# Performance work log

Measured on AMD Instinct MI355X. Metric: run time of the kernel, lower is better.

## Reference

```python
import jax, jax.numpy as jnp
import numpy as np
import math

H = 32           # num heads
D_NOPE = 128
D_ROPE = 64
D_V = 128
HID = 4096
FFN = 16384
SEQ = 2048
B = 1
ROPE_BASE = 10000.0
EPS = 1e-6


def _layernorm(x, w, b):
    mu = jnp.mean(x, axis=-1, keepdims=True)
    var = jnp.var(x, axis=-1, keepdims=True)
    return (x - mu) * jax.lax.rsqrt(var + EPS) * w + b


def _rope(x):
    # x: [B, S, H, D_ROPE]; standard half-split rotary, positions = arange(S)
    S = x.shape[1]
    half = D_ROPE // 2
    inv_freq = 1.0 / (ROPE_BASE ** (jnp.arange(0, D_ROPE, 2, dtype=jnp.float32) / D_ROPE))  # [half]
    t = jnp.arange(S, dtype=jnp.float32)
    freqs = t[:, None] * inv_freq[None, :]           # [S, half]
    cos = jnp.cos(freqs)[None, :, None, :]           # [1, S, 1, half]
    sin = jnp.sin(freqs)[None, :, None, :]
    x1, x2 = x[..., :half], x[..., half:]
    return jnp.concatenate([x1 * cos - x2 * sin, x1 * sin + x2 * cos], axis=-1)


def setup_inputs() -> dict:
    key = jax.random.key(0)
    ks = jax.random.split(key, 8)
    std = 0.02
    hidden_states = jax.random.normal(ks[0], (B, SEQ, HID), dtype=jnp.float32)
    # causal additive mask
    causal = jnp.triu(jnp.full((SEQ, SEQ), -1e9, dtype=jnp.float32), k=1)
    attention_mask = causal[None, None, :, :]
    q_size = H * (D_NOPE + D_ROPE)
    w_q = jax.random.normal(ks[1], (q_size, HID), dtype=jnp.float32) * std
    w_k = jax.random.normal(ks[2], (q_size, HID), dtype=jnp.float32) * std
    w_v = jax.random.normal(ks[3], (H * D_V, HID), dtype=jnp.float32) * std
    w_o = jax.random.normal(ks[4], (HID, H * D_V), dtype=jnp.float32) * std
    w1 = jax.random.normal(ks[5], (FFN, HID), dtype=jnp.float32) * std
    w2 = jax.random.normal(ks[6], (HID, FFN), dtype=jnp.float32) * std
    ln1_w = jnp.ones((HID,), jnp.float32); ln1_b = jnp.zeros((HID,), jnp.float32)
    ln2_w = jnp.ones((HID,), jnp.float32); ln2_b = jnp.zeros((HID,), jnp.float32)
    return dict(hidden_states=hidden_states, attention_mask=attention_mask,
                w_q=w_q, w_k=w_k, w_v=w_v, w_o=w_o,
                ln1_w=ln1_w, ln1_b=ln1_b, ln2_w=ln2_w, ln2_b=ln2_b,
                w1=w1, w2=w2)


def reference(hidden_states, attention_mask, w_q, w_k, w_v, w_o,
              ln1_w, ln1_b, ln2_w, ln2_b, w1, w2):
    x = hidden_states
    b, s, _ = x.shape
    # --- attention block ---
    h = _layernorm(x, ln1_w, ln1_b)
    q = h @ w_q.T   # [b, s, H*(nope+rope)]
    k = h @ w_k.T
    v = (h @ w_v.T).reshape(b, s, H, D_V)
    q_nope = q[..., :H * D_NOPE].reshape(b, s, H, D_NOPE)
    q_rope = q[..., H * D_NOPE:].reshape(b, s, H, D_ROPE)
    k_nope = k[..., :H * D_NOPE].reshape(b, s, H, D_NOPE)
    k_rope = k[..., H * D_NOPE:].reshape(b, s, H, D_ROPE)
    q_rope = _rope(q_rope)
    k_rope = _rope(k_rope)
    scores = (jnp.einsum('bqhd,bkhd->bhqk', q_nope, k_nope) / math.sqrt(D_NOPE)
              + jnp.einsum('bqhd,bkhd->bhqk', q_rope, k_rope) / math.sqrt(D_ROPE))
    scores = scores + attention_mask
    attn = jax.nn.softmax(scores, axis=-1)
    ctx = jnp.einsum('bhqk,bkhd->bqhd', attn, v).reshape(b, s, H * D_V)
    attn_out = ctx @ w_o.T
    x = x + attn_out
    # --- FFN block (silu MLP) ---
    h2 = _layernorm(x, ln2_w, ln2_b)
    ffn = jax.nn.silu(h2 @ w1.T) @ w2.T
    return x + ffn
```

## Files before the change

### kernel.cpp

```cpp
#include <hip/hip_runtime.h>

typedef _Float16 f16x8 __attribute__((ext_vector_type(8)));
typedef _Float16 f16x4 __attribute__((ext_vector_type(4)));
typedef float f32x4 __attribute__((ext_vector_type(4)));

#define HID 4096
#define QDIM 6144
#define SEQ 2048
#define NH 32

__global__ __launch_bounds__(256) void ln_k(const float* __restrict__ x,
    const float* __restrict__ w, const float* __restrict__ b,
    _Float16* __restrict__ out)
{
    __shared__ float red[8];
    const int tid = threadIdx.x;
    const int row = blockIdx.x;
    const float* xr = x + (size_t)row * HID;
    float4 v[4];
    float s = 0.f, ss = 0.f;
#pragma unroll
    for (int i = 0; i < 4; i++) {
        v[i] = ((const float4*)xr)[i * 256 + tid];
        s  += v[i].x + v[i].y + v[i].z + v[i].w;
        ss += v[i].x * v[i].x + v[i].y * v[i].y + v[i].z * v[i].z + v[i].w * v[i].w;
    }
#pragma unroll
    for (int o = 1; o < 64; o <<= 1) { s += __shfl_xor(s, o); ss += __shfl_xor(ss, o); }
    if ((tid & 63) == 0) { red[tid >> 6] = s; red[4 + (tid >> 6)] = ss; }
    __syncthreads();
    s  = red[0] + red[1] + red[2] + red[3];
    ss = red[4] + red[5] + red[6] + red[7];
    const float mu = s * (1.f / HID);
    const float rstd = rsqrtf(ss * (1.f / HID) - mu * mu + 1e-6f);
    _Float16* orow = out + (size_t)row * HID;
#pragma unroll
    for (int i = 0; i < 4; i++) {
        int base = (i * 256 + tid) * 4;
        float vv[4] = { v[i].x, v[i].y, v[i].z, v[i].w };
#pragma unroll
        for (int c = 0; c < 4; c++)
            orow[base + c] = (_Float16)((vv[c] - mu) * rstd * w[base + c] + b[base + c]);
    }
}

template<int EPI>
__global__ __launch_bounds__(256) void gemm_k(const _Float16* __restrict__ A,
    const float* __restrict__ W, int N, int K,
    _Float16* __restrict__ o16, const float* __restrict__ resid,
    float* __restrict__ of)
{
    __shared__ _Float16 As[128 * 40];
    __shared__ _Float16 Ws[128 * 40];
    const int tid  = threadIdx.x;
    const int lane = tid & 63, wid = tid >> 6;
    const int l15  = lane & 15, quad = lane >> 4;
    const int wr   = wid >> 1,  wc   = wid & 1;
    const int m0 = blockIdx.x * 128, n0 = blockIdx.y * 128;

    f32x4 acc[4][4] = {};
    for (int k0 = 0; k0 < K; k0 += 32) {
        __syncthreads();
#pragma unroll
        for (int it = 0, c = tid; it < 2; it++, c += 256) {
            int row = c >> 2, col = (c & 3) << 3;
            f16x8 v = *(const f16x8*)(A + (size_t)(m0 + row) * K + k0 + col);
            *(f16x8*)(As + row * 40 + col) = v;
        }
#pragma unroll
        for (int it = 0, c = tid; it < 4; it++, c += 256) {
            int row = c >> 3, col = (c & 7) << 2;
            float4 wv = *(const float4*)(W + (size_t)(n0 + row) * K + k0 + col);
            f16x4 hv = { (_Float16)wv.x, (_Float16)wv.y, (_Float16)wv.z, (_Float16)wv.w };
            *(f16x4*)(Ws + row * 40 + col) = hv;
        }
        __syncthreads();
        f16x8 a[4], b[4];
#pragma unroll
        for (int i = 0; i < 4; i++)
            a[i] = *(const f16x8*)(As + (wr * 64 + i * 16 + l15) * 40 + quad * 8);
#pragma unroll
        for (int j = 0; j < 4; j++)
            b[j] = *(const f16x8*)(Ws + (wc * 64 + j * 16 + l15) * 40 + quad * 8);
#pragma unroll
        for (int i = 0; i < 4; i++)
#pragma unroll
            for (int j = 0; j < 4; j++)
                acc[i][j] = __builtin_amdgcn_mfma_f32_16x16x32_f16(a[i], b[j], acc[i][j], 0, 0, 0);
    }
#pragma unroll
    for (int i = 0; i < 4; i++) {
#pragma unroll
        for (int j = 0; j < 4; j++) {
#pragma unroll
            for (int r = 0; r < 4; r++) {
                int rg = m0 + wr * 64 + i * 16 + quad * 4 + r;
                int cg = n0 + wc * 64 + j * 16 + l15;
                size_t idx = (size_t)rg * N + cg;
                float cv = acc[i][j][r];
                if (EPI == 0)      o16[idx] = (_Float16)cv;
                else if (EPI == 1) o16[idx] = (_Float16)(cv / (1.f + __expf(-cv)));
                else               of[idx]  = resid[idx] + cv;
            }
        }
    }
}

__global__ __launch_bounds__(256) void rope_k(_Float16* __restrict__ q,
                                              _Float16* __restrict__ k)
{
    const int s = blockIdx.x, tid = threadIdx.x;
    _Float16* qr = q + (size_t)s * QDIM;
    _Float16* kr = k + (size_t)s * QDIM;
    const float scn = 0.08838834764831845f;
#pragma unroll
    for (int it = 0, c = tid; it < 2; it++, c += 256) {
        f16x8 v = *(const f16x8*)(qr + c * 8);
#pragma unroll
        for (int e = 0; e < 8; e++) v[e] = (_Float16)((float)v[e] * scn);
        *(f16x8*)(qr + c * 8) = v;
    }
#pragma unroll
    for (int it = 0, c = tid; it < 4; it++, c += 256) {
        int hh = c >> 5, i = c & 31;
        float invf = exp2f(-(float)i * 0.41524101186092029f);
        float ang = (float)s * invf;
        float co = cosf(ang), si = sinf(ang);
        int base = HID + hh * 64 + i;
        {
            float x1 = (float)qr[base], x2 = (float)qr[base + 32];
            qr[base]      = (_Float16)((x1 * co - x2 * si) * 0.125f);
            qr[base + 32] = (_Float16)((x1 * si + x2 * co) * 0.125f);
        }
        {
            float x1 = (float)kr[base], x2 = (float)kr[base + 32];
            kr[base]      = (_Float16)(x1 * co - x2 * si);
            kr[base + 32] = (_Float16)(x1 * si + x2 * co);
        }
    }
}

__global__ __launch_bounds__(256) void attn_k(const _Float16* __restrict__ qb,
    const _Float16* __restrict__ kb, const _Float16* __restrict__ vb,
    _Float16* __restrict__ ctxb)
{
    __shared__ _Float16 Ks[64 * 200];
    __shared__ _Float16 Vt[128 * 72];
    __shared__ _Float16 Ps[4][16 * 72];
    const int q0 = blockIdx.x * 64;
    const int h  = blockIdx.y;
    const int tid = threadIdx.x, lane = tid & 63, wid = tid >> 6;
    const int l15 = lane & 15, quad = lane >> 4;

    f16x8 aq[6];
    {
        const _Float16* qrow = qb + (size_t)(q0 + wid * 16 + l15) * QDIM;
#pragma unroll
        for (int c = 0; c < 6; c++) {
            int colb = (c < 4) ? (h * 128 + c * 32) : (HID + h * 64 + (c - 4) * 32);
            aq[c] = *(const f16x8*)(qrow + colb + quad * 8);
        }
    }
    f32x4 oacc[8] = {};
    float mrun[4] = { -1e30f, -1e30f, -1e30f, -1e30f };
    float lrun[4] = { 0.f, 0.f, 0.f, 0.f };

    const int nk = blockIdx.x + 1;
    for (int kt = 0; kt < nk; kt++) {
        const int k0 = kt * 64;
        __syncthreads();
        for (int c = tid; c < 1536; c += 256) {
            int f8 = c % 24, row = c / 24;
            int f = f8 << 3;
            int col = (f < 128) ? (h * 128 + f) : (HID + h * 64 + (f - 128));
            f16x8 v = *(const f16x8*)(kb + (size_t)(k0 + row) * QDIM + col);
            *(f16x8*)(Ks + row * 200 + f) = v;
        }
        for (int c = tid; c < 1024; c += 256) {
            int kl = c & 63, d8 = c >> 6;
            f16x8 v = *(const f16x8*)(vb + (size_t)(k0 + kl) * HID + h * 128 + (d8 << 3));
#pragma unroll
            for (int e = 0; e < 8; e++) Vt[(d8 * 8 + e) * 72 + kl] = v[e];
        }
        __syncthreads();
        f32x4 sa[4];
#pragma unroll
        for (int nt = 0; nt < 4; nt++) {
            f32x4 acc = {};
#pragma unroll
            for (int c = 0; c < 6; c++) {
                f16x8 bk = *(const f16x8*)(Ks + (nt * 16 + l15) * 200 + c * 32 + quad * 8);
                acc = __builtin_amdgcn_mfma_f32_16x16x32_f16(aq[c], bk, acc, 0, 0, 0);
            }
            sa[nt] = acc;
        }
#pragma unroll
        for (int r = 0; r < 4; r++) {
            const int qrow = q0 + wid * 16 + quad * 4 + r;
            float mx = -1e30f;
#pragma unroll
            for (int nt = 0; nt < 4; nt++) {
                int kcol = k0 + nt * 16 + l15;
                float sv = (kcol <= qrow) ? sa[nt][r] : -1e30f;
                sa[nt][r] = sv;
                mx = fmaxf(mx, sv);
            }
#pragma unroll
            for (int o = 1; o < 16; o <<= 1) mx = fmaxf(mx, __shfl_xor(mx, o));
            float mnew = fmaxf(mrun[r], mx);
            float alpha = __expf(mrun[r] - mnew);
            mrun[r] = mnew;
            float sum = 0.f;
#pragma unroll
            for (int nt = 0; nt < 4; nt++) {
                float p = __expf(sa[nt][r] - mnew);
                sa[nt][r] = p;
                sum += p;
            }
#pragma unroll
            for (int o = 1; o < 16; o <<= 1) sum += __shfl_xor(sum, o);
            lrun[r] = lrun[r] * alpha + sum;
#pragma unroll
            for (int ot = 0; ot < 8; ot++) oacc[ot][r] *= alpha;
#pragma unroll
            for (int nt = 0; nt < 4; nt++)
                Ps[wid][(quad * 4 + r) * 72 + nt * 16 + l15] = (_Float16)sa[nt][r];
        }
#pragma unroll
        for (int kc = 0; kc < 2; kc++) {
            f16x8 ap = *(const f16x8*)(&Ps[wid][l15 * 72 + kc * 32 + quad * 8]);
#pragma unroll
            for (int ot = 0; ot < 8; ot++) {
                f16x8 bv = *(const f16x8*)(Vt + (ot * 16 + l15) * 72 + kc * 32 + quad * 8);
                oacc[ot] = __builtin_amdgcn_mfma_f32_16x16x32_f16(ap, bv, oacc[ot], 0, 0, 0);
            }
        }
    }
#pragma unroll
    for (int r = 0; r < 4; r++) {
        const int srow = q0 + wid * 16 + quad * 4 + r;
        const float inv = 1.0f / lrun[r];
#pragma unroll
        for (int ot = 0; ot < 8; ot++)
            ctxb[(size_t)srow * HID + h * 128 + ot * 16 + l15] = (_Float16)(oacc[ot][r] * inv);
    }
}

extern "C" void kernel_launch(void* const* d_in, const int* in_sizes, int n_in,
                              void* d_out, int out_size, void* d_ws, size_t ws_size,
                              hipStream_t stream)
{
    const float* x   = (const float*)d_in[0];
    const float* wq  = (const float*)d_in[2];
    const float* wk  = (const float*)d_in[3];
    const float* wv  = (const float*)d_in[4];
    const float* wo  = (const float*)d_in[5];
    const float* l1w = (const float*)d_in[6];
    const float* l1b = (const float*)d_in[7];
    const float* l2w = (const float*)d_in[8];
    const float* l2b = (const float*)d_in[9];
    const float* w1  = (const float*)d_in[10];
    const float* w2  = (const float*)d_in[11];
    float* out = (float*)d_out;

    _Float16* ws   = (_Float16*)d_ws;
    _Float16* hb   = ws;
    _Float16* qb   = ws + 8388608;
    _Float16* kb   = qb + 12582912;
    _Float16* vb   = kb + 12582912;
    _Float16* ctxb = vb + 8388608;
    _Float16* h2b  = hb;
    _Float16* f1b  = qb;

    ln_k<<<SEQ, 256, 0, stream>>>(x, l1w, l1b, hb);
    gemm_k<0><<<dim3(16, 48),  256, 0, stream>>>(hb, wq, QDIM, HID, qb, nullptr, nullptr);
    gemm_k<0><<<dim3(16, 48),  256, 0, stream>>>(hb, wk, QDIM, HID, kb, nullptr, nullptr);
    gemm_k<0><<<dim3(16, 32),  256, 0, stream>>>(hb, wv, HID,  HID, vb, nullptr, nullptr);
    rope_k<<<SEQ, 256, 0, stream>>>(qb, kb);
    attn_k<<<dim3(32, NH), 256, 0, stream>>>(qb, kb, vb, ctxb);
    gemm_k<2><<<dim3(16, 32),  256, 0, stream>>>(ctxb, wo, HID, HID, nullptr, x, out);
    ln_k<<<SEQ, 256, 0, stream>>>(out, l2w, l2b, h2b);
    gemm_k<1><<<dim3(16, 128), 256, 0, stream>>>(h2b, w1, 16384, HID, f1b, nullptr, nullptr);
    gemm_k<2><<<dim3(16, 32),  256, 0, stream>>>(f1b, w2, HID, 16384, nullptr, out, out);
}
```

Before: 2.715 ms.

## Pre-convert weights to fp16, fuse QKV GEMM, use direct-to-LDS loads with swizzle

When the workspace is large enough, weights are converted to fp16 in separate kernels and Q/K/V are computed by one fused GEMM into an interleaved QKV buffer. The GEMM now uses global_load_lds direct-to-LDS copies with an XOR swizzle, a K-step of 64, and an XCD-aware block remapping. Otherwise it reads fp32 weights into LDS and converts on read. The goal is to cut the per-tile fp32 conversion and register staging overhead, at the cost of extra conversion passes over the weights each call.

```diff
diff --git a/kernel.cpp b/kernel.cpp
--- a/kernel.cpp
+++ b/kernel.cpp
@@ -5,9 +5,25 @@
 typedef float f32x4 __attribute__((ext_vector_type(4)));
 
 #define HID 4096
-#define QDIM 6144
 #define SEQ 2048
 #define NH 32
+#define QKVS 16384
+
+__device__ __forceinline__ void load_lds16(const void* g, void* l) {
+    __builtin_amdgcn_global_load_lds((const __attribute__((address_space(1))) void*)g,
+                                     (__attribute__((address_space(3))) void*)l, 16, 0, 0);
+}
+
+__global__ __launch_bounds__(256) void conv_k(const float* __restrict__ s,
+                                              _Float16* __restrict__ d)
+{
+    size_t i = ((size_t)blockIdx.x * 256 + threadIdx.x) * 8;
+    float4 a = *(const float4*)(s + i);
+    float4 b = *(const float4*)(s + i + 4);
+    f16x8 o = { (_Float16)a.x, (_Float16)a.y, (_Float16)a.z, (_Float16)a.w,
+                (_Float16)b.x, (_Float16)b.y, (_Float16)b.z, (_Float16)b.w };
+    *(f16x8*)(d + i) = o;
+}
 
 __global__ __launch_bounds__(256) void ln_k(const float* __restrict__ x,
     const float* __restrict__ w, const float* __restrict__ b,
@@ -44,81 +60,118 @@
     }
 }
 
-template<int EPI>
+template<int EPI, bool WF32>
 __global__ __launch_bounds__(256) void gemm_k(const _Float16* __restrict__ A,
-    const float* __restrict__ W, int N, int K,
+    const _Float16* __restrict__ W16, const float* __restrict__ W32,
+    int N, int K, int ldc,
     _Float16* __restrict__ o16, const float* __restrict__ resid,
     float* __restrict__ of)
 {
-    __shared__ _Float16 As[128 * 40];
-    __shared__ _Float16 Ws[128 * 40];
+    __shared__ _Float16 As[128 * 64];
+    __shared__ _Float16 Ws16[WF32 ? 8 : 128 * 64];
+    __shared__ float    Ws32[WF32 ? 128 * 64 : 8];
+
     const int tid  = threadIdx.x;
     const int lane = tid & 63, wid = tid >> 6;
     const int l15  = lane & 15, quad = lane >> 4;
     const int wr   = wid >> 1,  wc   = wid & 1;
-    const int m0 = blockIdx.x * 128, n0 = blockIdx.y * 128;
+
+    const int Nblk = gridDim.y;
+    const int lin  = blockIdx.y * 16 + blockIdx.x;
+    const int xcd  = lin & 7, sl = lin >> 3;
+    const int mb   = (xcd >> 2) * 8 + (sl & 7);
+    const int nb   = (xcd & 3) * (Nblk >> 2) + (sl >> 3);
+    const int m0 = mb * 128, n0 = nb * 128;
+
+    const int srow  = lane >> 3;
+    const int sblk  = (lane & 7) ^ (srow & 7);
+    const _Float16* gA = A + (size_t)(m0 + wid * 32 + srow) * K + sblk * 8;
+    const int srow32 = lane >> 4;
+    const _Float16* gB16 = WF32 ? nullptr
+        : W16 + (size_t)(n0 + wid * 32 + srow) * K + sblk * 8;
 
     f32x4 acc[4][4] = {};
-    for (int k0 = 0; k0 < K; k0 += 32) {
+    for (int k0 = 0; k0 < K; k0 += 64) {
         __syncthreads();
 #pragma unroll
-        for (int it = 0, c = tid; it < 2; it++, c += 256) {
-            int row = c >> 2, col = (c & 3) << 3;
-            f16x8 v = *(const f16x8*)(A + (size_t)(m0 + row) * K + k0 + col);
-            *(f16x8*)(As + row * 40 + col) = v;
-        }
-#pragma unroll
-        for (int it = 0, c = tid; it < 4; it++, c += 256) {
-            int row = c >> 3, col = (c & 7) << 2;
-            float4 wv = *(const float4*)(W + (size_t)(n0 + row) * K + k0 + col);
-            f16x4 hv = { (_Float16)wv.x, (_Float16)wv.y, (_Float16)wv.z, (_Float16)wv.w };
-            *(f16x4*)(Ws + row * 40 + col) = hv;
+        for (int i = 0; i < 4; i++)
+            load_lds16(gA + (size_t)i * 8 * K + k0, As + (wid * 32 + i * 8) * 64);
+        if constexpr (!WF32) {
+#pragma unroll
+            for (int i = 0; i < 4; i++)
+                load_lds16(gB16 + (size_t)i * 8 * K + k0, Ws16 + (wid * 32 + i * 8) * 64);
+        } else {
+#pragma unroll
+            for (int i = 0; i < 8; i++) {
+                int bg = (lane & 15) ^ (((i & 3) << 2) | srow32);
+                const float* g = W32 + (size_t)(n0 + wid * 32 + i * 4 + srow32) * K + k0 + bg * 4;
+                load_lds16(g, Ws32 + (wid * 32 + i * 4) * 64);
+            }
         }
         __syncthreads();
-        f16x8 a[4], b[4];
-#pragma unroll
-        for (int i = 0; i < 4; i++)
-            a[i] = *(const f16x8*)(As + (wr * 64 + i * 16 + l15) * 40 + quad * 8);
+
+        f16x8 a[2][4], b[2][4];
+#pragma unroll
+        for (int kk = 0; kk < 2; kk++)
+#pragma unroll
+            for (int i = 0; i < 4; i++)
+                a[kk][i] = *(const f16x8*)(As + (wr * 64 + i * 16 + l15) * 64 +
+                                           (((kk << 2) + quad) ^ (l15 & 7)) * 8);
+#pragma unroll
+        for (int kk = 0; kk < 2; kk++)
+#pragma unroll
+            for (int j = 0; j < 4; j++) {
+                if constexpr (!WF32) {
+                    b[kk][j] = *(const f16x8*)(Ws16 + (wc * 64 + j * 16 + l15) * 64 +
+                                               (((kk << 2) + quad) ^ (l15 & 7)) * 8);
+                } else {
+                    const float* base = Ws32 + (wc * 64 + j * 16 + l15) * 64;
+                    int p0 = ((kk << 2) + quad) << 1;
+                    f32x4 w0 = *(const f32x4*)(base + ((p0 ^ l15) << 2));
+                    f32x4 w1 = *(const f32x4*)(base + (((p0 + 1) ^ l15) << 2));
+#pragma unroll
+                    for (int e = 0; e < 4; e++) {
+                        b[kk][j][e]     = (_Float16)w0[e];
+                        b[kk][j][4 + e] = (_Float16)w1[e];
+                    }
+                }
+            }
+#pragma unroll
+        for (int kk = 0; kk < 2; kk++)
+#pragma unroll
+            for (int i = 0; i < 4; i++)
+#pragma unroll
+                for (int j = 0; j < 4; j++)
+                    acc[i][j] = __builtin_amdgcn_mfma_f32_16x16x32_f16(a[kk][i], b[kk][j], acc[i][j], 0, 0, 0);
+    }
+
+#pragma unroll
+    for (int i = 0; i < 4; i++)
 #pragma unroll
         for (int j = 0; j < 4; j++)
-            b[j] = *(const f16x8*)(Ws + (wc * 64 + j * 16 + l15) * 40 + quad * 8);
-#pragma unroll
-        for (int i = 0; i < 4; i++)
-#pragma unroll
-            for (int j = 0; j < 4; j++)
-                acc[i][j] = __builtin_amdgcn_mfma_f32_16x16x32_f16(a[i], b[j], acc[i][j], 0, 0, 0);
-    }
-#pragma unroll
-    for (int i = 0; i < 4; i++) {
-#pragma unroll
-        for (int j = 0; j < 4; j++) {
 #pragma unroll
             for (int r = 0; r < 4; r++) {
                 int rg = m0 + wr * 64 + i * 16 + quad * 4 + r;
                 int cg = n0 + wc * 64 + j * 16 + l15;
-                size_t idx = (size_t)rg * N + cg;
+                size_t idx = (size_t)rg * ldc + cg;
                 float cv = acc[i][j][r];
                 if (EPI == 0)      o16[idx] = (_Float16)cv;
                 else if (EPI == 1) o16[idx] = (_Float16)(cv / (1.f + __expf(-cv)));
                 else               of[idx]  = resid[idx] + cv;
             }
-        }
-    }
-}
-
-__global__ __launch_bounds__(256) void rope_k(_Float16* __restrict__ q,
-                                              _Float16* __restrict__ k)
+}
+
+__global__ __launch_bounds__(256) void rope_k(_Float16* __restrict__ qkv)
 {
     const int s = blockIdx.x, tid = threadIdx.x;
-    _Float16* qr = q + (size_t)s * QDIM;
-    _Float16* kr = k + (size_t)s * QDIM;
+    _Float16* row = qkv + (size_t)s * QKVS;
     const float scn = 0.08838834764831845f;
 #pragma unroll
     for (int it = 0, c = tid; it < 2; it++, c += 256) {
-        f16x8 v = *(const f16x8*)(qr + c * 8);
+        f16x8 v = *(const f16x8*)(row + c * 8);
 #pragma unroll
         for (int e = 0; e < 8; e++) v[e] = (_Float16)((float)v[e] * scn);
-        *(f16x8*)(qr + c * 8) = v;
+        *(f16x8*)(row + c * 8) = v;
     }
 #pragma unroll
     for (int it = 0, c = tid; it < 4; it++, c += 256) {
@@ -126,23 +179,23 @@
         float invf = exp2f(-(float)i * 0.41524101186092029f);
         float ang = (float)s * invf;
         float co = cosf(ang), si = sinf(ang);
-        int base = HID + hh * 64 + i;
+        int qb = 4096 + hh * 64 + i;
+        int kb = 10240 + hh * 64 + i;
         {
-            float x1 = (float)qr[base], x2 = (float)qr[base + 32];
-            qr[base]      = (_Float16)((x1 * co - x2 * si) * 0.125f);
-            qr[base + 32] = (_Float16)((x1 * si + x2 * co) * 0.125f);
+            float x1 = (float)row[qb], x2 = (float)row[qb + 32];
+            row[qb]      = (_Float16)((x1 * co - x2 * si) * 0.125f);
+            row[qb + 32] = (_Float16)((x1 * si + x2 * co) * 0.125f);
         }
         {
-            float x1 = (float)kr[base], x2 = (float)kr[base + 32];
-            kr[base]      = (_Float16)(x1 * co - x2 * si);
-            kr[base + 32] = (_Float16)(x1 * si + x2 * co);
-        }
-    }
-}
-
-__global__ __launch_bounds__(256) void attn_k(const _Float16* __restrict__ qb,
-    const _Float16* __restrict__ kb, const _Float16* __restrict__ vb,
-    _Float16* __restrict__ ctxb)
+            float x1 = (float)row[kb], x2 = (float)row[kb + 32];
+            row[kb]      = (_Float16)(x1 * co - x2 * si);
+            row[kb + 32] = (_Float16)(x1 * si + x2 * co);
+        }
+    }
+}
+
+__global__ __launch_bounds__(256) void attn_k(const _Float16* __restrict__ qkv,
+                                              _Float16* __restrict__ ctxb)
 {
     __shared__ _Float16 Ks[64 * 200];
     __shared__ _Float16 Vt[128 * 72];
@@ -151,13 +204,16 @@
     const int h  = blockIdx.y;
     const int tid = threadIdx.x, lane = tid & 63, wid = tid >> 6;
     const int l15 = lane & 15, quad = lane >> 4;
+    const _Float16* qb = qkv;
+    const _Float16* kb = qkv + 6144;
+    const _Float16* vb = qkv + 12288;
 
     f16x8 aq[6];
     {
-        const _Float16* qrow = qb + (size_t)(q0 + wid * 16 + l15) * QDIM;
+        const _Float16* qrow = qb + (size_t)(q0 + wid * 16 + l15) * QKVS;
 #pragma unroll
         for (int c = 0; c < 6; c++) {
-            int colb = (c < 4) ? (h * 128 + c * 32) : (HID + h * 64 + (c - 4) * 32);
+            int colb = (c < 4) ? (h * 128 + c * 32) : (4096 + h * 64 + (c - 4) * 32);
             aq[c] = *(const f16x8*)(qrow + colb + quad * 8);
         }
     }
@@ -170,15 +226,15 @@
         const int k0 = kt * 64;
         __syncthreads();
         for (int c = tid; c < 1536; c += 256) {
-            int f8 = c % 24, row = c / 24;
+            int f8 = c % 24, r = c / 24;
             int f = f8 << 3;
-            int col = (f < 128) ? (h * 128 + f) : (HID + h * 64 + (f - 128));
-            f16x8 v = *(const f16x8*)(kb + (size_t)(k0 + row) * QDIM + col);
-            *(f16x8*)(Ks + row * 200 + f) = v;
+            int col = (f < 128) ? (h * 128 + f) : (4096 + h * 64 + (f - 128));
+            f16x8 v = *(const f16x8*)(kb + (size_t)(k0 + r) * QKVS + col);
+            *(f16x8*)(Ks + r * 200 + f) = v;
         }
         for (int c = tid; c < 1024; c += 256) {
             int kl = c & 63, d8 = c >> 6;
-            f16x8 v = *(const f16x8*)(vb + (size_t)(k0 + kl) * HID + h * 128 + (d8 << 3));
+            f16x8 v = *(const f16x8*)(vb + (size_t)(k0 + kl) * QKVS + h * 128 + (d8 << 3));
 #pragma unroll
             for (int e = 0; e < 8; e++) Vt[(d8 * 8 + e) * 72 + kl] = v[e];
         }
@@ -262,24 +318,43 @@
     const float* w1  = (const float*)d_in[10];
     const float* w2  = (const float*)d_in[11];
     float* out = (float*)d_out;
-
-    _Float16* ws   = (_Float16*)d_ws;
-    _Float16* hb   = ws;
-    _Float16* qb   = ws + 8388608;
-    _Float16* kb   = qb + 12582912;
-    _Float16* vb   = kb + 12582912;
-    _Float16* ctxb = vb + 8388608;
-    _Float16* h2b  = hb;
-    _Float16* f1b  = qb;
-
-    ln_k<<<SEQ, 256, 0, stream>>>(x, l1w, l1b, hb);
-    gemm_k<0><<<dim3(16, 48),  256, 0, stream>>>(hb, wq, QDIM, HID, qb, nullptr, nullptr);
-    gemm_k<0><<<dim3(16, 48),  256, 0, stream>>>(hb, wk, QDIM, HID, kb, nullptr, nullptr);
-    gemm_k<0><<<dim3(16, 32),  256, 0, stream>>>(hb, wv, HID,  HID, vb, nullptr, nullptr);
-    rope_k<<<SEQ, 256, 0, stream>>>(qb, kb);
-    attn_k<<<dim3(32, NH), 256, 0, stream>>>(qb, kb, vb, ctxb);
-    gemm_k<2><<<dim3(16, 32),  256, 0, stream>>>(ctxb, wo, HID, HID, nullptr, x, out);
-    ln_k<<<SEQ, 256, 0, stream>>>(out, l2w, l2b, h2b);
-    gemm_k<1><<<dim3(16, 128), 256, 0, stream>>>(h2b, w1, 16384, HID, f1b, nullptr, nullptr);
-    gemm_k<2><<<dim3(16, 32),  256, 0, stream>>>(f1b, w2, HID, 16384, nullptr, out, out);
-}
+    _Float16* ws = (_Float16*)d_ws;
+
+    if (ws_size >= (size_t)268435456) {
+        _Float16* Wb   = ws;
+        _Float16* Wo16 = ws + 67108864;
+        _Float16* hb   = ws + 83886080;
+        _Float16* qkvb = ws + 92274688;
+        _Float16* ctx  = ws + 125829120;
+
+        conv_k<<<12288, 256, 0, stream>>>(wq, Wb);
+        conv_k<<<12288, 256, 0, stream>>>(wk, Wb + 25165824);
+        conv_k<<<8192,  256, 0, stream>>>(wv, Wb + 50331648);
+        conv_k<<<8192,  256, 0, stream>>>(wo, Wo16);
+        ln_k<<<SEQ, 256, 0, stream>>>(x, l1w, l1b, hb);
+        gemm_k<0, false><<<dim3(16, 128), 256, 0, stream>>>(hb, Wb, nullptr, 16384, 4096, QKVS, qkvb, nullptr, nullptr);
+        rope_k<<<SEQ, 256, 0, stream>>>(qkvb);
+        attn_k<<<dim3(32, NH), 256, 0, stream>>>(qkvb, ctx);
+        gemm_k<2, false><<<dim3(16, 32), 256, 0, stream>>>(ctx, Wo16, nullptr, 4096, 4096, 4096, nullptr, x, out);
+        ln_k<<<SEQ, 256, 0, stream>>>(out, l2w, l2b, hb);
+        conv_k<<<32768, 256, 0, stream>>>(w1, Wb);
+        gemm_k<1, false><<<dim3(16, 128), 256, 0, stream>>>(hb, Wb, nullptr, 16384, 4096, QKVS, qkvb, nullptr, nullptr);
+        conv_k<<<32768, 256, 0, stream>>>(w2, Wb);
+        gemm_k<2, false><<<dim3(16, 32), 256, 0, stream>>>(qkvb, Wb, nullptr, 4096, 16384, 4096, nullptr, out, out);
+    } else {
+        _Float16* hb   = ws;
+        _Float16* qkvb = ws + 8388608;
+        _Float16* ctx  = ws + 41943040;
+
+        ln_k<<<SEQ, 256, 0, stream>>>(x, l1w, l1b, hb);
+        gemm_k<0, true><<<dim3(16, 48), 256, 0, stream>>>(hb, nullptr, wq, 6144, 4096, QKVS, qkvb, nullptr, nullptr);
+        gemm_k<0, true><<<dim3(16, 48), 256, 0, stream>>>(hb, nullptr, wk, 6144, 4096, QKVS, qkvb + 6144, nullptr, nullptr);
+        gemm_k<0, true><<<dim3(16, 32), 256, 0, stream>>>(hb, nullptr, wv, 4096, 4096, QKVS, qkvb + 12288, nullptr, nullptr);
+        rope_k<<<SEQ, 256, 0, stream>>>(qkvb);
+        attn_k<<<dim3(32, NH), 256, 0, stream>>>(qkvb, ctx);
+        gemm_k<2, true><<<dim3(16, 32), 256, 0, stream>>>(ctx, nullptr, wo, 4096, 4096, 4096, nullptr, x, out);
+        ln_k<<<SEQ, 256, 0, stream>>>(out, l2w, l2b, hb);
+        gemm_k<1, true><<<dim3(16, 128), 256, 0, stream>>>(hb, nullptr, w1, 16384, 4096, QKVS, qkvb, nullptr, nullptr);
+        gemm_k<2, true><<<dim3(16, 32), 256, 0, stream>>>(qkvb, nullptr, w2, 4096, 16384, 4096, nullptr, out, out);
+    }
+}
```

Result: faster. 2.187 ms (-19.4%).
